# Kernel tuning notes

Measured on AMD Instinct MI355X. Metric: run time of the kernel, lower is better.

## Reference

```python
import jax, jax.numpy as jnp
import numpy as np
from jax import lax

H = 128          # hidden_size
D = 8            # input_size
GX, GY = 4, 4    # grid_size
C = GX * GY      # grid cells
NS = 4.0         # neighborhood_size
T = 15           # obs_len
N = 16384        # neighbors per frame


def setup_inputs() -> dict:
    key = jax.random.key(0)
    ks = jax.random.split(key, 30)
    def w(i, shape):
        return jax.random.normal(ks[i], shape, jnp.float32) * 0.05
    return {
        "observed_trajectory_target": jax.random.normal(ks[0], (T, D), jnp.float32),
        "observed_trajectory_others": jax.random.normal(ks[1], (T, N, D), jnp.float32),
        "neighbor_mask": jax.random.randint(ks[2], (T, N), 0, 2, dtype=jnp.int32),
        "W_ih": w(3, (4 * H, D)), "W_hh": w(4, (4 * H, H)),
        "b_ih": w(5, (4 * H,)), "b_hh": w(6, (4 * H,)),
        "Wq": w(7, (H, H)), "bq": w(8, (H,)),
        "Wk": w(9, (H, H)), "bk": w(10, (H,)),
        "Wv": w(11, (H, H)), "bv": w(12, (H,)),
        "Wo": w(13, (H, H)), "bo": w(14, (H,)),
        "Wgq": w(15, (H, H)), "bgq": w(16, (H,)),
        "Wgk": w(17, (H, H)), "bgk": w(18, (H,)),
        "Wgv": w(19, (H, H)), "bgv": w(20, (H,)),
        "Wc": w(21, (2, H)), "bc": w(22, (2,)),
    }


def _lstm_cell(x, h, c, W_ih, W_hh, b_ih, b_hh):
    # torch LSTMCell gate order: i, f, g, o
    g = x @ W_ih.T + b_ih + h @ W_hh.T + b_hh
    i, f, gg, o = jnp.split(g, 4, axis=-1)
    c2 = jax.nn.sigmoid(f) * c + jax.nn.sigmoid(i) * jnp.tanh(gg)
    h2 = jax.nn.sigmoid(o) * jnp.tanh(c2)
    return h2, c2


def _forward(target, others, mask, W_ih, W_hh, b_ih, b_hh, Wq, bq, Wk, bk, Wv, bv,
             Wo, bo, Wgq, bgq, Wgk, bgk, Wgv, bgv, Wc, bc):
    # Neighbor LSTM is re-initialized to zero every timestep in the original
    # -> single LSTM step from zero state, vectorized over [T, N].
    g = jnp.einsum('tnd,kd->tnk', others, W_ih) + b_ih + b_hh
    i, f, gg, o = jnp.split(g, 4, axis=-1)
    c_o = jax.nn.sigmoid(i) * jnp.tanh(gg)
    h_others = jax.nn.sigmoid(o) * jnp.tanh(c_o)          # [T, N, H]

    scale = 1.0 / jnp.sqrt(jnp.asarray(H, jnp.float32))
    half = NS / 2.0
    cw, ch = NS / GX, NS / GY
    cells = jnp.arange(C, dtype=jnp.int32)

    def step(carry, xs):
        h, c = carry
        xt, ho, pos, mk = xs                               # [D], [N,H], [N,2], [N]
        h, c = _lstm_cell(xt[None, :], h, c, W_ih, W_hh, b_ih, b_hh)  # [1,H]
        # --- dynamic grid binning (trunc-toward-zero matches torch .long()) ---
        rel = pos - xt[:2]                                 # [N,2]
        in_nb = (jnp.abs(rel[:, 0]) <= half) & (jnp.abs(rel[:, 1]) <= half)
        cx = jnp.trunc(rel[:, 0] / cw).astype(jnp.int32) + GX // 2
        cy = jnp.trunc(rel[:, 1] / ch).astype(jnp.int32) + GY // 2
        valid = in_nb & (cx >= 0) & (cx < GX) & (cy >= 0) & (cy < GY) & (mk != 0)
        idx = cy * GX + cx                                 # [N]
        member = (idx[None, :] == cells[:, None]) & valid[None, :]  # [C,N]
        # --- per-cell single-query attention (1-head MHA) ---
        q = h @ Wq.T + bq                                  # [1,H]
        k = ho @ Wk.T + bk                                 # [N,H]
        v = ho @ Wv.T + bv                                 # [N,H]
        sc = (q @ k.T)[0] * scale                          # [N]
        mx = jnp.max(jnp.where(member, sc[None, :], -1e30), axis=1, keepdims=True)
        e = jnp.where(member, jnp.exp(sc[None, :] - mx), 0.0)
        w = e / jnp.maximum(e.sum(axis=1, keepdims=True), 1e-30)  # [C,N]
        nonempty = member.any(axis=1)                      # [C]
        cell_out = (w @ v) @ Wo.T + bo                     # [C,H]
        cell_out = jnp.where(nonempty[:, None], cell_out, 0.0)  # empty cells -> exact zeros
        # --- grid-level attention over the C cell summaries ---
        K = cell_out @ Wgk.T + bgk                         # [C,H]
        V = cell_out @ Wgv.T + bgv                         # [C,H]
        qg = h @ Wgq.T + bgq                               # [1,H]
        gw = jax.nn.softmax((qg @ K.T) * scale, axis=-1)   # [1,C]
        ctx = gw @ V                                       # [1,H]
        combined = h + ctx                                 # [1,H]
        return (h, c), combined

    h0 = jnp.zeros((1, H), jnp.float32)
    c0 = jnp.zeros((1, H), jnp.float32)
    _, ys = lax.scan(step, (h0, c0),
                     (target, h_others, others[..., :2], mask))
    combined = ys[-1][None]                                # [1,1,H] (matches torch broadcast)
    return combined @ Wc.T + bc                            # [1,1,2]


def reference(observed_trajectory_target, observed_trajectory_others, neighbor_mask,
              W_ih, W_hh, b_ih, b_hh, Wq, bq, Wk, bk, Wv, bv, Wo, bo,
              Wgq, bgq, Wgk, bgk, Wgv, bgv, Wc, bc):
    return _forward(observed_trajectory_target, observed_trajectory_others, neighbor_mask,
                    W_ih, W_hh, b_ih, b_hh, Wq, bq, Wk, bk, Wv, bv, Wo, bo,
                    Wgq, bgq, Wgk, bgk, Wgv, bgv, Wc, bc)
```

## Files before the change

### kernel.cpp

```cpp
#include <hip/hip_runtime.h>
#include <math.h>

#define WS_H    0
#define WS_U    128
#define WS_W2   256
#define WS_QBK  384
#define WS_S0   385
#define WS_S1   386
#define WS_ACC  512
#define WS_ESUM 2560

__device__ __forceinline__ float frcp_(float x){ return __builtin_amdgcn_rcpf(x); }
__device__ __forceinline__ float fsig_(float x){ return frcp_(1.f + __expf(-x)); }
__device__ __forceinline__ float ftanh_(float x){ return 1.f - 2.f*frcp_(1.f + __expf(2.f*x)); }

__global__ __launch_bounds__(512) void k1_target(
    const float* __restrict__ target,
    const float* __restrict__ W_ih, const float* __restrict__ W_hh,
    const float* __restrict__ b_ih, const float* __restrict__ b_hh,
    const float* __restrict__ Wq,  const float* __restrict__ bq,
    const float* __restrict__ Wk,  const float* __restrict__ bk,
    const float* __restrict__ Wv,  const float* __restrict__ bv,
    const float* __restrict__ Wo,  const float* __restrict__ bo,
    const float* __restrict__ Wgq, const float* __restrict__ bgq,
    const float* __restrict__ Wgk, const float* __restrict__ bgk,
    float* __restrict__ ws)
{
    __shared__ __align__(16) float h_s[128];
    __shared__ float g_s[512];
    __shared__ __align__(16) float q_s[128], qg_s[128], u_s[128], ug_s[128], w1_s[128], w2_s[128];
    __shared__ float red[384];
    const int tid = threadIdx.x;

    for (int i = tid; i < 16*128 + 16; i += 512) ws[WS_ACC + i] = 0.f;
    if (tid < 128) h_s[tid] = 0.f;

    float wih[8];
    #pragma unroll
    for (int k = 0; k < 8; ++k) wih[k] = W_ih[tid*8 + k];
    const float bsum = b_ih[tid] + b_hh[tid];
    float4 whh[32];
    {
        const float4* w4 = (const float4*)(W_hh + tid*128);
        #pragma unroll
        for (int m = 0; m < 32; ++m) whh[m] = w4[m];
    }
    float c = 0.f;
    __syncthreads();

    for (int t = 0; t < 15; ++t) {
        float g = bsum;
        #pragma unroll
        for (int k = 0; k < 8; ++k) g += target[t*8 + k] * wih[k];
        const float4* h4 = (const float4*)h_s;
        float acc = 0.f;
        #pragma unroll
        for (int m = 0; m < 32; ++m) {
            float4 hv = h4[m];
            acc += whh[m].x*hv.x + whh[m].y*hv.y + whh[m].z*hv.z + whh[m].w*hv.w;
        }
        g += acc;
        g_s[tid] = g;
        __syncthreads();
        if (tid < 128) {
            float ig = fsig_(g_s[tid]);
            float fg = fsig_(g_s[tid+128]);
            float gg = ftanh_(g_s[tid+256]);
            float og = fsig_(g_s[tid+384]);
            c = fg*c + ig*gg;
            h_s[tid] = og*ftanh_(c);
        }
        __syncthreads();
    }

    if (tid < 128) {
        const float4* wq4  = (const float4*)(Wq  + tid*128);
        const float4* wgq4 = (const float4*)(Wgq + tid*128);
        const float4* h4 = (const float4*)h_s;
        float a1 = bq[tid], a2 = bgq[tid];
        #pragma unroll
        for (int m = 0; m < 32; ++m) {
            float4 hv = h4[m]; float4 wa = wq4[m]; float4 wb = wgq4[m];
            a1 += wa.x*hv.x + wa.y*hv.y + wa.z*hv.z + wa.w*hv.w;
            a2 += wb.x*hv.x + wb.y*hv.y + wb.z*hv.z + wb.w*hv.w;
        }
        q_s[tid] = a1; qg_s[tid] = a2;
    }
    __syncthreads();
    if (tid < 128) {
        float a1 = 0.f, a2 = 0.f;
        for (int j = 0; j < 128; ++j) {
            a1 += q_s[j]  * Wk[j*128 + tid];
            a2 += qg_s[j] * Wgk[j*128 + tid];
        }
        u_s[tid] = a1; ug_s[tid] = a2;
    }
    __syncthreads();
    if (tid < 128) {
        float a = 0.f;
        for (int j = 0; j < 128; ++j) a += ug_s[j] * Wo[j*128 + tid];
        w1_s[tid] = a;
    }
    __syncthreads();
    if (tid < 128) {
        float a = 0.f;
        for (int j = 0; j < 128; ++j) a += w1_s[j] * Wv[j*128 + tid];
        w2_s[tid] = a;
        red[tid]     = q_s[tid]*bk[tid];
        red[128+tid] = qg_s[tid]*bgk[tid];
        red[256+tid] = w1_s[tid]*bv[tid] + ug_s[tid]*bo[tid];
    }
    __syncthreads();
    if (tid == 0) {
        float qbk = 0.f, s0 = 0.f, sx = 0.f;
        for (int j = 0; j < 128; ++j) { qbk += red[j]; s0 += red[128+j]; sx += red[256+j]; }
        ws[WS_QBK] = qbk; ws[WS_S0] = s0; ws[WS_S1] = sx + s0;
    }
    if (tid < 128) {
        ws[WS_H + tid]  = h_s[tid];
        ws[WS_U + tid]  = u_s[tid];
        ws[WS_W2 + tid] = w2_s[tid];
    }
}

#define K3_BLOCKS 128
__global__ __launch_bounds__(256) void k3_neighbors(
    const float* __restrict__ target, const float* __restrict__ others,
    const int* __restrict__ mask, const float* __restrict__ W_ih,
    const float* __restrict__ b_ih, const float* __restrict__ b_hh,
    float* __restrict__ ws)
{
    __shared__ float accs[16*128];
    __shared__ float esums[16];
    __shared__ int used[16];
    const int tid  = threadIdx.x;
    const int lane = tid & 63;
    const int wave = tid >> 6;

    for (int i = tid; i < 2048; i += 256) accs[i] = 0.f;
    if (tid < 16) { esums[tid] = 0.f; used[tid] = 0; }

    const int d0 = lane, d1 = lane + 64;
    float wi0[8], wg0[8], wo0[8], wi1[8], wg1[8], wo1[8];
    #pragma unroll
    for (int k = 0; k < 8; ++k) {
        wi0[k] = W_ih[d0*8+k];        wi1[k] = W_ih[d1*8+k];
        wg0[k] = W_ih[(256+d0)*8+k];  wg1[k] = W_ih[(256+d1)*8+k];
        wo0[k] = W_ih[(384+d0)*8+k];  wo1[k] = W_ih[(384+d1)*8+k];
    }
    const float bi0 = b_ih[d0]+b_hh[d0],         bi1 = b_ih[d1]+b_hh[d1];
    const float bg0 = b_ih[256+d0]+b_hh[256+d0], bg1 = b_ih[256+d1]+b_hh[256+d1];
    const float bo0 = b_ih[384+d0]+b_hh[384+d0], bo1 = b_ih[384+d1]+b_hh[384+d1];
    const float u0 = ws[WS_U + d0], u1 = ws[WS_U + d1];
    const float qbk = ws[WS_QBK];
    const float tx0 = target[14*8 + 0], tx1 = target[14*8 + 1];
    const float* __restrict__ oth  = others + 14*16384*8;
    const int*   __restrict__ mk14 = mask   + 14*16384;
    const float scale = 0.08838834764831845f;
    __syncthreads();

    const int gw = blockIdx.x*4 + wave;
    const int nper = 16384 / (K3_BLOCKS*4);
    for (int n = gw*nper; n < gw*nper + nper; ++n) {
        const int mk = mk14[n];
        const float4 xa = ((const float4*)oth)[n*2];
        const float4 xb = ((const float4*)oth)[n*2 + 1];
        const float r0 = xa.x - tx0, r1 = xa.y - tx1;
        bool ok = (fabsf(r0) <= 2.f) & (fabsf(r1) <= 2.f) & (mk != 0);
        const int cx = (int)truncf(r0) + 2;
        const int cy = (int)truncf(r1) + 2;
        ok = ok & (cx >= 0) & (cx < 4) & (cy >= 0) & (cy < 4);
        if (!ok) continue;
        const int cell = cy*4 + cx;
        float x[8] = {xa.x, xa.y, xa.z, xa.w, xb.x, xb.y, xb.z, xb.w};
        float gi = bi0, gg = bg0, go = bo0;
        #pragma unroll
        for (int k = 0; k < 8; ++k) { gi += x[k]*wi0[k]; gg += x[k]*wg0[k]; go += x[k]*wo0[k]; }
        const float ho0 = fsig_(go) * ftanh_(fsig_(gi) * ftanh_(gg));
        gi = bi1; gg = bg1; go = bo1;
        #pragma unroll
        for (int k = 0; k < 8; ++k) { gi += x[k]*wi1[k]; gg += x[k]*wg1[k]; go += x[k]*wo1[k]; }
        const float ho1 = fsig_(go) * ftanh_(fsig_(gi) * ftanh_(gg));
        float p = u0*ho0 + u1*ho1;
        #pragma unroll
        for (int s = 1; s < 64; s <<= 1) p += __shfl_xor(p, s, 64);
        const float sc = (p + qbk) * scale;
        const float e = __expf(sc);
        atomicAdd(&accs[cell*128 + d0], e*ho0);
        atomicAdd(&accs[cell*128 + d1], e*ho1);
        if (lane == 0) { atomicAdd(&esums[cell], e); used[cell] = 1; }
    }
    __syncthreads();
    for (int i = tid; i < 2048; i += 256) {
        const int c = i >> 7;
        if (used[c]) {
            const float v = accs[i];
            if (v != 0.f) atomicAdd(&ws[WS_ACC + i], v);
        }
    }
    if (tid < 16 && used[tid]) atomicAdd(&ws[WS_ESUM + tid], esums[tid]);
}

__global__ __launch_bounds__(128) void k4_finale(
    const float* __restrict__ Wv, const float* __restrict__ bv,
    const float* __restrict__ Wo, const float* __restrict__ bo,
    const float* __restrict__ Wgv, const float* __restrict__ bgv,
    const float* __restrict__ Wc, const float* __restrict__ bc,
    const float* __restrict__ ws, float* __restrict__ out)
{
    __shared__ __align__(16) float avg[16*128];
    __shared__ float gw_s[16];
    __shared__ float s_sh[16];
    __shared__ __align__(16) float mavg[128], t_s[128], mix[128], comb[128];
    __shared__ float alpha_s;
    const int tid = threadIdx.x;
    const float scale = 0.08838834764831845f;

    #pragma unroll
    for (int c = 0; c < 16; ++c) {
        const float es = ws[WS_ESUM + c];
        avg[c*128 + tid] = (es > 0.f) ? ws[WS_ACC + c*128 + tid] / es : 0.f;
    }
    __syncthreads();
    if (tid < 16) {
        const float es = ws[WS_ESUM + tid];
        float s;
        if (es > 0.f) {
            s = ws[WS_S1];
            for (int m = 0; m < 128; ++m) s += ws[WS_W2 + m] * avg[tid*128 + m];
        } else {
            s = ws[WS_S0];
        }
        s_sh[tid] = s * scale;
    }
    __syncthreads();
    if (tid == 0) {
        float mx = -1e30f;
        #pragma unroll
        for (int c = 0; c < 16; ++c) mx = fmaxf(mx, s_sh[c]);
        float e[16]; float den = 0.f;
        #pragma unroll
        for (int c = 0; c < 16; ++c) { e[c] = __expf(s_sh[c] - mx); den += e[c]; }
        float a = 0.f;
        #pragma unroll
        for (int c = 0; c < 16; ++c) {
            const float g = e[c] / den;
            gw_s[c] = g;
            if (ws[WS_ESUM + c] > 0.f) a += g;
        }
        alpha_s = a;
    }
    __syncthreads();
    {
        float a = 0.f;
        #pragma unroll
        for (int c = 0; c < 16; ++c) a += gw_s[c] * avg[c*128 + tid];
        mavg[tid] = a;
    }
    __syncthreads();
    const float alpha = alpha_s;
    {
        float a = alpha * bv[tid];
        const float4* w = (const float4*)(Wv + tid*128);
        const float4* v = (const float4*)mavg;
        #pragma unroll
        for (int m = 0; m < 32; ++m) { float4 ww = w[m], vv = v[m];
            a += ww.x*vv.x + ww.y*vv.y + ww.z*vv.z + ww.w*vv.w; }
        t_s[tid] = a;
    }
    __syncthreads();
    {
        float a = alpha * bo[tid];
        const float4* w = (const float4*)(Wo + tid*128);
        const float4* v = (const float4*)t_s;
        #pragma unroll
        for (int m = 0; m < 32; ++m) { float4 ww = w[m], vv = v[m];
            a += ww.x*vv.x + ww.y*vv.y + ww.z*vv.z + ww.w*vv.w; }
        mix[tid] = a;
    }
    __syncthreads();
    {
        float a = bgv[tid];
        const float4* w = (const float4*)(Wgv + tid*128);
        const float4* v = (const float4*)mix;
        #pragma unroll
        for (int m = 0; m < 32; ++m) { float4 ww = w[m], vv = v[m];
            a += ww.x*vv.x + ww.y*vv.y + ww.z*vv.z + ww.w*vv.w; }
        comb[tid] = ws[WS_H + tid] + a;
    }
    __syncthreads();
    if (tid < 2) {
        float a = bc[tid];
        for (int m = 0; m < 128; ++m) a += Wc[tid*128 + m] * comb[m];
        out[tid] = a;
    }
}

extern "C" void kernel_launch(void* const* d_in, const int* in_sizes, int n_in,
                              void* d_out, int out_size, void* d_ws, size_t ws_size,
                              hipStream_t stream) {
    (void)in_sizes; (void)n_in; (void)out_size; (void)ws_size;
    const float* target = (const float*)d_in[0];
    const float* others = (const float*)d_in[1];
    const int*   mask   = (const int*)d_in[2];
    const float* W_ih = (const float*)d_in[3];
    const float* W_hh = (const float*)d_in[4];
    const float* b_ih = (const float*)d_in[5];
    const float* b_hh = (const float*)d_in[6];
    const float* Wq  = (const float*)d_in[7];  const float* bq  = (const float*)d_in[8];
    const float* Wk  = (const float*)d_in[9];  const float* bk  = (const float*)d_in[10];
    const float* Wv  = (const float*)d_in[11]; const float* bv  = (const float*)d_in[12];
    const float* Wo  = (const float*)d_in[13]; const float* bo  = (const float*)d_in[14];
    const float* Wgq = (const float*)d_in[15]; const float* bgq = (const float*)d_in[16];
    const float* Wgk = (const float*)d_in[17]; const float* bgk = (const float*)d_in[18];
    const float* Wgv = (const float*)d_in[19]; const float* bgv = (const float*)d_in[20];
    const float* Wc  = (const float*)d_in[21]; const float* bc  = (const float*)d_in[22];
    float* ws  = (float*)d_ws;
    float* out = (float*)d_out;

    k1_target<<<dim3(1), dim3(512), 0, stream>>>(target, W_ih, W_hh, b_ih, b_hh,
        Wq, bq, Wk, bk, Wv, bv, Wo, bo, Wgq, bgq, Wgk, bgk, ws);
    k3_neighbors<<<dim3(K3_BLOCKS), dim3(256), 0, stream>>>(target, others, mask,
        W_ih, b_ih, b_hh, ws);
    k4_finale<<<dim3(1), dim3(128), 0, stream>>>(Wv, bv, Wo, bo, Wgv, bgv, Wc, bc, ws, out);
}
```

Baseline: 174.0 us.

## Add cache-warming prefetch kernel, parallelize target matvecs, replicate accumulators

```diff
diff --git a/kernel.cpp b/kernel.cpp
--- a/kernel.cpp
+++ b/kernel.cpp
@@ -1,20 +1,57 @@
 #include <hip/hip_runtime.h>
 #include <math.h>
 
-#define WS_H    0
-#define WS_U    128
-#define WS_W2   256
-#define WS_QBK  384
-#define WS_S0   385
-#define WS_S1   386
-#define WS_ACC  512
-#define WS_ESUM 2560
+#define WS_H     0
+#define WS_U     128
+#define WS_W2    256
+#define WS_QBK   384
+#define WS_S0    385
+#define WS_S1    386
+#define WS_GUARD 400
+#define WS_ACCR  512
+#define REP_STRIDE 2064
+#define NREP 4
 
 __device__ __forceinline__ float frcp_(float x){ return __builtin_amdgcn_rcpf(x); }
 __device__ __forceinline__ float fsig_(float x){ return frcp_(1.f + __expf(-x)); }
 __device__ __forceinline__ float ftanh_(float x){ return 1.f - 2.f*frcp_(1.f + __expf(2.f*x)); }
 
-__global__ __launch_bounds__(512) void k1_target(
+__device__ __forceinline__ float pf_(const float* __restrict__ p, int n, int part, int tid) {
+    const int per4 = n >> 7;
+    const float4* p4 = (const float4*)p + part * per4;
+    float a = 0.f;
+    for (int i = tid; i < per4; i += 256) { float4 v = p4[i]; a += v.x + v.y + v.z + v.w; }
+    return a;
+}
+
+__global__ __launch_bounds__(256) void k0_prefetch(
+    const float* __restrict__ W_ih, const float* __restrict__ W_hh,
+    const float* __restrict__ Wq,  const float* __restrict__ Wk,
+    const float* __restrict__ Wv,  const float* __restrict__ Wo,
+    const float* __restrict__ Wgq, const float* __restrict__ Wgk,
+    const float* __restrict__ Wgv, const float* __restrict__ Wc,
+    float* __restrict__ ws)
+{
+    const int tid = threadIdx.x;
+    const int bid = blockIdx.x;
+    if (bid == 0) {
+        for (int i = tid; i < NREP * REP_STRIDE; i += 256) ws[WS_ACCR + i] = 0.f;
+    }
+    const int part = bid >> 3;
+    float a = pf_(W_hh, 65536, part, tid);
+    a += pf_(W_ih, 4096,  part, tid);
+    a += pf_(Wq,  16384, part, tid);
+    a += pf_(Wk,  16384, part, tid);
+    a += pf_(Wv,  16384, part, tid);
+    a += pf_(Wo,  16384, part, tid);
+    a += pf_(Wgq, 16384, part, tid);
+    a += pf_(Wgk, 16384, part, tid);
+    a += pf_(Wgv, 16384, part, tid);
+    if (part < 2) a += pf_(Wc, 256, part, tid);
+    if (a == 1.0e38f) ws[WS_GUARD] = a;
+}
+
+__global__ __launch_bounds__(512, 2) void k1_target(
     const float* __restrict__ target,
     const float* __restrict__ W_ih, const float* __restrict__ W_hh,
     const float* __restrict__ b_ih, const float* __restrict__ b_hh,
@@ -28,11 +65,10 @@
 {
     __shared__ __align__(16) float h_s[128];
     __shared__ float g_s[512];
-    __shared__ __align__(16) float q_s[128], qg_s[128], u_s[128], ug_s[128], w1_s[128], w2_s[128];
-    __shared__ float red[384];
+    __shared__ float red[512];
+    __shared__ __align__(16) float qq_s[256];
+    __shared__ __align__(16) float u_s[128], ug_s[128], w1_s[128], w2_s[128];
     const int tid = threadIdx.x;
-
-    for (int i = tid; i < 16*128 + 16; i += 512) ws[WS_ACC + i] = 0.f;
     if (tid < 128) h_s[tid] = 0.f;
 
     float wih[8];
@@ -53,13 +89,16 @@
         #pragma unroll
         for (int k = 0; k < 8; ++k) g += target[t*8 + k] * wih[k];
         const float4* h4 = (const float4*)h_s;
-        float acc = 0.f;
-        #pragma unroll
-        for (int m = 0; m < 32; ++m) {
-            float4 hv = h4[m];
-            acc += whh[m].x*hv.x + whh[m].y*hv.y + whh[m].z*hv.z + whh[m].w*hv.w;
-        }
-        g += acc;
+        float a0 = 0.f, a1 = 0.f, a2 = 0.f, a3 = 0.f;
+        #pragma unroll
+        for (int m = 0; m < 32; m += 4) {
+            float4 x0 = h4[m], x1 = h4[m+1], x2 = h4[m+2], x3 = h4[m+3];
+            a0 += whh[m  ].x*x0.x + whh[m  ].y*x0.y + whh[m  ].z*x0.z + whh[m  ].w*x0.w;
+            a1 += whh[m+1].x*x1.x + whh[m+1].y*x1.y + whh[m+1].z*x1.z + whh[m+1].w*x1.w;
+            a2 += whh[m+2].x*x2.x + whh[m+2].y*x2.y + whh[m+2].z*x2.z + whh[m+2].w*x2.w;
+            a3 += whh[m+3].x*x3.x + whh[m+3].y*x3.y + whh[m+3].z*x3.z + whh[m+3].w*x3.w;
+        }
+        g += (a0 + a1) + (a2 + a3);
         g_s[tid] = g;
         __syncthreads();
         if (tid < 128) {
@@ -73,41 +112,59 @@
         __syncthreads();
     }
 
+    {
+        const int o = tid & 255, p = tid >> 8;
+        const float* Wrow = (o < 128) ? (Wq + o*128) : (Wgq + (o & 127)*128);
+        const float4* w4 = (const float4*)Wrow + p*16;
+        const float4* h4 = (const float4*)h_s + p*16;
+        float a = 0.f;
+        #pragma unroll
+        for (int m = 0; m < 16; ++m) { float4 w = w4[m], v = h4[m];
+            a += w.x*v.x + w.y*v.y + w.z*v.z + w.w*v.w; }
+        red[tid] = a;
+    }
+    __syncthreads();
+    if (tid < 256) qq_s[tid] = red[tid] + red[tid+256] + ((tid < 128) ? bq[tid] : bgq[tid & 127]);
+    __syncthreads();
+    {
+        const int o = tid & 255, p = tid >> 8;
+        const int a_ = o & 127;
+        const float* W = (o < 128) ? Wk : Wgk;
+        const int qb = (o < 128) ? 0 : 128;
+        float a = 0.f;
+        #pragma unroll 8
+        for (int j = p*64; j < p*64 + 64; ++j) a += qq_s[qb + j] * W[j*128 + a_];
+        red[tid] = a;
+    }
+    __syncthreads();
+    if (tid < 256) {
+        float v = red[tid] + red[tid+256];
+        if (tid < 128) u_s[tid] = v; else ug_s[tid & 127] = v;
+    }
+    __syncthreads();
+    {
+        const int o = tid & 127, p = tid >> 7;
+        float a = 0.f;
+        #pragma unroll 8
+        for (int j = p*32; j < p*32 + 32; ++j) a += ug_s[j] * Wo[j*128 + o];
+        red[tid] = a;
+    }
+    __syncthreads();
+    if (tid < 128) w1_s[tid] = red[tid] + red[tid+128] + red[tid+256] + red[tid+384];
+    __syncthreads();
+    {
+        const int o = tid & 127, p = tid >> 7;
+        float a = 0.f;
+        #pragma unroll 8
+        for (int j = p*32; j < p*32 + 32; ++j) a += w1_s[j] * Wv[j*128 + o];
+        red[tid] = a;
+    }
+    __syncthreads();
+    if (tid < 128) w2_s[tid] = red[tid] + red[tid+128] + red[tid+256] + red[tid+384];
+    __syncthreads();
     if (tid < 128) {
-        const float4* wq4  = (const float4*)(Wq  + tid*128);
-        const float4* wgq4 = (const float4*)(Wgq + tid*128);
-        const float4* h4 = (const float4*)h_s;
-        float a1 = bq[tid], a2 = bgq[tid];
-        #pragma unroll
-        for (int m = 0; m < 32; ++m) {
-            float4 hv = h4[m]; float4 wa = wq4[m]; float4 wb = wgq4[m];
-            a1 += wa.x*hv.x + wa.y*hv.y + wa.z*hv.z + wa.w*hv.w;
-            a2 += wb.x*hv.x + wb.y*hv.y + wb.z*hv.z + wb.w*hv.w;
-        }
-        q_s[tid] = a1; qg_s[tid] = a2;
-    }
-    __syncthreads();
-    if (tid < 128) {
-        float a1 = 0.f, a2 = 0.f;
-        for (int j = 0; j < 128; ++j) {
-            a1 += q_s[j]  * Wk[j*128 + tid];
-            a2 += qg_s[j] * Wgk[j*128 + tid];
-        }
-        u_s[tid] = a1; ug_s[tid] = a2;
-    }
-    __syncthreads();
-    if (tid < 128) {
-        float a = 0.f;
-        for (int j = 0; j < 128; ++j) a += ug_s[j] * Wo[j*128 + tid];
-        w1_s[tid] = a;
-    }
-    __syncthreads();
-    if (tid < 128) {
-        float a = 0.f;
-        for (int j = 0; j < 128; ++j) a += w1_s[j] * Wv[j*128 + tid];
-        w2_s[tid] = a;
-        red[tid]     = q_s[tid]*bk[tid];
-        red[128+tid] = qg_s[tid]*bgk[tid];
+        red[tid]     = qq_s[tid] * bk[tid];
+        red[128+tid] = qq_s[128+tid] * bgk[tid];
         red[256+tid] = w1_s[tid]*bv[tid] + ug_s[tid]*bo[tid];
     }
     __syncthreads();
@@ -123,7 +180,7 @@
     }
 }
 
-#define K3_BLOCKS 128
+#define K3_BLOCKS 64
 __global__ __launch_bounds__(256) void k3_neighbors(
     const float* __restrict__ target, const float* __restrict__ others,
     const int* __restrict__ mask, const float* __restrict__ W_ih,
@@ -191,14 +248,16 @@
         if (lane == 0) { atomicAdd(&esums[cell], e); used[cell] = 1; }
     }
     __syncthreads();
+    const int rep = blockIdx.x & (NREP-1);
+    float* wacc = ws + WS_ACCR + rep*REP_STRIDE;
     for (int i = tid; i < 2048; i += 256) {
         const int c = i >> 7;
         if (used[c]) {
             const float v = accs[i];
-            if (v != 0.f) atomicAdd(&ws[WS_ACC + i], v);
-        }
-    }
-    if (tid < 16 && used[tid]) atomicAdd(&ws[WS_ESUM + tid], esums[tid]);
+            if (v != 0.f) atomicAdd(&wacc[i], v);
+        }
+    }
+    if (tid < 16 && used[tid]) atomicAdd(&wacc[2048 + tid], esums[tid]);
 }
 
 __global__ __launch_bounds__(128) void k4_finale(
@@ -209,6 +268,7 @@
     const float* __restrict__ ws, float* __restrict__ out)
 {
     __shared__ __align__(16) float avg[16*128];
+    __shared__ float es_s[16];
     __shared__ float gw_s[16];
     __shared__ float s_sh[16];
     __shared__ __align__(16) float mavg[128], t_s[128], mix[128], comb[128];
@@ -216,16 +276,24 @@
     const int tid = threadIdx.x;
     const float scale = 0.08838834764831845f;
 
+    if (tid < 16) {
+        float e = 0.f;
+        #pragma unroll
+        for (int r = 0; r < NREP; ++r) e += ws[WS_ACCR + r*REP_STRIDE + 2048 + tid];
+        es_s[tid] = e;
+    }
+    __syncthreads();
     #pragma unroll
     for (int c = 0; c < 16; ++c) {
-        const float es = ws[WS_ESUM + c];
-        avg[c*128 + tid] = (es > 0.f) ? ws[WS_ACC + c*128 + tid] / es : 0.f;
+        float a = 0.f;
+        #pragma unroll
+        for (int r = 0; r < NREP; ++r) a += ws[WS_ACCR + r*REP_STRIDE + c*128 + tid];
+        avg[c*128 + tid] = (es_s[c] > 0.f) ? a / es_s[c] : 0.f;
     }
     __syncthreads();
     if (tid < 16) {
-        const float es = ws[WS_ESUM + tid];
         float s;
-        if (es > 0.f) {
+        if (es_s[tid] > 0.f) {
             s = ws[WS_S1];
             for (int m = 0; m < 128; ++m) s += ws[WS_W2 + m] * avg[tid*128 + m];
         } else {
@@ -246,7 +314,7 @@
         for (int c = 0; c < 16; ++c) {
             const float g = e[c] / den;
             gw_s[c] = g;
-            if (ws[WS_ESUM + c] > 0.f) a += g;
+            if (es_s[c] > 0.f) a += g;
         }
         alpha_s = a;
     }
@@ -318,6 +386,8 @@
     float* ws  = (float*)d_ws;
     float* out = (float*)d_out;
 
+    k0_prefetch<<<dim3(256), dim3(256), 0, stream>>>(W_ih, W_hh, Wq, Wk, Wv, Wo,
+        Wgq, Wgk, Wgv, Wc, ws);
     k1_target<<<dim3(1), dim3(512), 0, stream>>>(target, W_ih, W_hh, b_ih, b_hh,
         Wq, bq, Wk, bk, Wv, bv, Wo, bo, Wgq, bgq, Wgk, bgk, ws);
     k3_neighbors<<<dim3(K3_BLOCKS), dim3(256), 0, stream>>>(target, others, mask,
```

After: 189.1 us. 1.09x slower.
